# Kernel tuning notes

Hardware: AMD Instinct MI355X
Metric: run time of the kernel (lower is better)

Reference implementation:

```python
import jax, jax.numpy as jnp
import numpy as np

NUM_CLASSES = 1000
EMBED_DIM = 1024
BATCH = 32768
FACTOR = 0.3


def setup_inputs() -> dict:
    key = jax.random.key(0)
    k1, k2, k3 = jax.random.split(key, 3)
    embed = jax.random.normal(k1, (BATCH, EMBED_DIM), dtype=jnp.float32)
    y = jax.random.randint(k2, (BATCH,), 0, NUM_CLASSES, dtype=jnp.int64)
    centroid = jax.random.normal(k3, (NUM_CLASSES, EMBED_DIM), dtype=jnp.float32)
    return {"embed": embed, "y": y, "centroid": centroid}


def reference(embed, y, centroid):
    # Per-class sum of embeddings: equivalent to eye(C)[y].T @ embed,
    # done as a scatter-add (segment_sum) instead of a dense one-hot matmul.
    sums = jax.ops.segment_sum(embed, y, num_segments=NUM_CLASSES)  # [C, D]
    counts = jax.ops.segment_sum(
        jnp.ones((embed.shape[0],), dtype=embed.dtype), y, num_segments=NUM_CLASSES
    )  # [C] == weight.sum(dim=1)
    cur_centroid = sums / counts[:, None]  # per-class mean
    new_centroid = FACTOR * cur_centroid + (1.0 - FACTOR) * centroid
    return new_centroid
```

## Files before the change

kernel.cpp:

```cpp
#include <hip/hip_runtime.h>


#define BATCH       32768
#define EMBED_DIM   1024
#define NUM_CLASSES 1000
#define FACTOR      0.3f
#define MAX_ROWS    512

__global__ __launch_bounds__(256) void centroid_kernel(
    const float* __restrict__ embed,
    const int*   __restrict__ y,
    const float* __restrict__ centroid,
    float*       __restrict__ out)
{
    const int c   = blockIdx.x;
    const int tid = threadIdx.x;
    const int d0  = tid * 4;

    __shared__ int rows[MAX_ROWS];
    __shared__ int nmatch;

    if (tid == 0) nmatch = 0;

    const size_t o = (size_t)c * EMBED_DIM + d0;
    const float4 cen = *reinterpret_cast<const float4*>(centroid + o);

    __syncthreads();

    #pragma unroll 4
    for (int base = 0; base < BATCH; base += 1024) {
        const int idx = base + d0;
        const int4 v = *reinterpret_cast<const int4*>(y + idx);
        if (v.x == c) { int p = atomicAdd(&nmatch, 1); rows[p] = idx + 0; }
        if (v.y == c) { int p = atomicAdd(&nmatch, 1); rows[p] = idx + 1; }
        if (v.z == c) { int p = atomicAdd(&nmatch, 1); rows[p] = idx + 2; }
        if (v.w == c) { int p = atomicAdd(&nmatch, 1); rows[p] = idx + 3; }
    }
    __syncthreads();

    const int m = nmatch;

    float4 acc = make_float4(0.f, 0.f, 0.f, 0.f);
    int j = 0;
    for (; j + 8 <= m; j += 8) {
        float4 v[8];
        #pragma unroll
        for (int u = 0; u < 8; ++u) {
            const int r = rows[j + u];
            v[u] = *reinterpret_cast<const float4*>(
                embed + (size_t)r * EMBED_DIM + d0);
        }
        #pragma unroll
        for (int u = 0; u < 8; ++u) {
            acc.x += v[u].x; acc.y += v[u].y;
            acc.z += v[u].z; acc.w += v[u].w;
        }
    }
    for (; j < m; ++j) {
        const int r = rows[j];
        const float4 v = *reinterpret_cast<const float4*>(
            embed + (size_t)r * EMBED_DIM + d0);
        acc.x += v.x; acc.y += v.y; acc.z += v.z; acc.w += v.w;
    }

    const float inv = 1.0f / (float)m;
    float4 res;
    res.x = FACTOR * (acc.x * inv) + (1.0f - FACTOR) * cen.x;
    res.y = FACTOR * (acc.y * inv) + (1.0f - FACTOR) * cen.y;
    res.z = FACTOR * (acc.z * inv) + (1.0f - FACTOR) * cen.z;
    res.w = FACTOR * (acc.w * inv) + (1.0f - FACTOR) * cen.w;
    *reinterpret_cast<float4*>(out + o) = res;
}

extern "C" void kernel_launch(void* const* d_in, const int* in_sizes, int n_in,
                              void* d_out, int out_size, void* d_ws, size_t ws_size,
                              hipStream_t stream) {
    const float* embed    = (const float*)d_in[0];
    const int*   y        = (const int*)d_in[1];
    const float* centroid = (const float*)d_in[2];
    float*       out      = (float*)d_out;

    centroid_kernel<<<NUM_CLASSES, 256, 0, stream>>>(embed, y, centroid, out);
}
```

Measured before the change: 211.7 us.

## Process four classes per block to amortize label scan

Each block now scans the label array once and buckets matching rows for four consecutive classes into per-class shared lists. It then gathers and averages each class in turn. This cuts the number of full label-array scans by four, reducing redundant L2 traffic. The trade-off is a quarter as many blocks, which lowers occupancy and concurrency during the embedding gather.

```diff
diff --git a/kernel.cpp b/kernel.cpp
--- a/kernel.cpp
+++ b/kernel.cpp
@@ -5,7 +5,8 @@
 #define EMBED_DIM   1024
 #define NUM_CLASSES 1000
 #define FACTOR      0.3f
-#define MAX_ROWS    512
+#define G           4
+#define MAXR        256
 
 __global__ __launch_bounds__(256) void centroid_kernel(
     const float* __restrict__ embed,
@@ -13,63 +14,65 @@
     const float* __restrict__ centroid,
     float*       __restrict__ out)
 {
-    const int c   = blockIdx.x;
+    const int c0  = blockIdx.x * G;
     const int tid = threadIdx.x;
     const int d0  = tid * 4;
 
-    __shared__ int rows[MAX_ROWS];
-    __shared__ int nmatch;
+    __shared__ int rows[G][MAXR];
+    __shared__ int nm[G];
 
-    if (tid == 0) nmatch = 0;
-
-    const size_t o = (size_t)c * EMBED_DIM + d0;
-    const float4 cen = *reinterpret_cast<const float4*>(centroid + o);
-
+    if (tid < G) nm[tid] = 0;
     __syncthreads();
 
-    #pragma unroll 4
+    #pragma unroll 8
     for (int base = 0; base < BATCH; base += 1024) {
         const int idx = base + d0;
         const int4 v = *reinterpret_cast<const int4*>(y + idx);
-        if (v.x == c) { int p = atomicAdd(&nmatch, 1); rows[p] = idx + 0; }
-        if (v.y == c) { int p = atomicAdd(&nmatch, 1); rows[p] = idx + 1; }
-        if (v.z == c) { int p = atomicAdd(&nmatch, 1); rows[p] = idx + 2; }
-        if (v.w == c) { int p = atomicAdd(&nmatch, 1); rows[p] = idx + 3; }
+        unsigned u;
+        u = (unsigned)(v.x - c0); if (u < G) { int p = atomicAdd(&nm[u], 1); rows[u][p] = idx + 0; }
+        u = (unsigned)(v.y - c0); if (u < G) { int p = atomicAdd(&nm[u], 1); rows[u][p] = idx + 1; }
+        u = (unsigned)(v.z - c0); if (u < G) { int p = atomicAdd(&nm[u], 1); rows[u][p] = idx + 2; }
+        u = (unsigned)(v.w - c0); if (u < G) { int p = atomicAdd(&nm[u], 1); rows[u][p] = idx + 3; }
     }
     __syncthreads();
 
-    const int m = nmatch;
+    for (int g = 0; g < G; ++g) {
+        const int m = nm[g];
+        const int* rl = rows[g];
 
-    float4 acc = make_float4(0.f, 0.f, 0.f, 0.f);
-    int j = 0;
-    for (; j + 8 <= m; j += 8) {
-        float4 v[8];
-        #pragma unroll
-        for (int u = 0; u < 8; ++u) {
-            const int r = rows[j + u];
-            v[u] = *reinterpret_cast<const float4*>(
+        float4 acc = make_float4(0.f, 0.f, 0.f, 0.f);
+        int j = 0;
+        for (; j + 8 <= m; j += 8) {
+            float4 v[8];
+            #pragma unroll
+            for (int u = 0; u < 8; ++u) {
+                const int r = rl[j + u];
+                v[u] = *reinterpret_cast<const float4*>(
+                    embed + (size_t)r * EMBED_DIM + d0);
+            }
+            #pragma unroll
+            for (int u = 0; u < 8; ++u) {
+                acc.x += v[u].x; acc.y += v[u].y;
+                acc.z += v[u].z; acc.w += v[u].w;
+            }
+        }
+        for (; j < m; ++j) {
+            const int r = rl[j];
+            const float4 v = *reinterpret_cast<const float4*>(
                 embed + (size_t)r * EMBED_DIM + d0);
+            acc.x += v.x; acc.y += v.y; acc.z += v.z; acc.w += v.w;
         }
-        #pragma unroll
-        for (int u = 0; u < 8; ++u) {
-            acc.x += v[u].x; acc.y += v[u].y;
-            acc.z += v[u].z; acc.w += v[u].w;
-        }
+
+        const float inv = 1.0f / (float)m;
+        const size_t o = (size_t)(c0 + g) * EMBED_DIM + d0;
+        const float4 cen = *reinterpret_cast<const float4*>(centroid + o);
+        float4 res;
+        res.x = FACTOR * (acc.x * inv) + (1.0f - FACTOR) * cen.x;
+        res.y = FACTOR * (acc.y * inv) + (1.0f - FACTOR) * cen.y;
+        res.z = FACTOR * (acc.z * inv) + (1.0f - FACTOR) * cen.z;
+        res.w = FACTOR * (acc.w * inv) + (1.0f - FACTOR) * cen.w;
+        *reinterpret_cast<float4*>(out + o) = res;
     }
-    for (; j < m; ++j) {
-        const int r = rows[j];
-        const float4 v = *reinterpret_cast<const float4*>(
-            embed + (size_t)r * EMBED_DIM + d0);
-        acc.x += v.x; acc.y += v.y; acc.z += v.z; acc.w += v.w;
-    }
-
-    const float inv = 1.0f / (float)m;
-    float4 res;
-    res.x = FACTOR * (acc.x * inv) + (1.0f - FACTOR) * cen.x;
-    res.y = FACTOR * (acc.y * inv) + (1.0f - FACTOR) * cen.y;
-    res.z = FACTOR * (acc.z * inv) + (1.0f - FACTOR) * cen.z;
-    res.w = FACTOR * (acc.w * inv) + (1.0f - FACTOR) * cen.w;
-    *reinterpret_cast<float4*>(out + o) = res;
 }
 
 extern "C" void kernel_launch(void* const* d_in, const int* in_sizes, int n_in,
@@ -80,5 +83,5 @@
     const float* centroid = (const float*)d_in[2];
     float*       out      = (float*)d_out;
 
-    centroid_kernel<<<NUM_CLASSES, 256, 0, stream>>>(embed, y, centroid, out);
+    centroid_kernel<<<NUM_CLASSES / G, 256, 0, stream>>>(embed, y, centroid, out);
 }
```

After: 217.3 us. +2.7%, slower.

## Split each class across two blocks over embedding halves with padded unrolled gather

Applied to the files above, without the earlier changes.

Launches two blocks per class, each handling half of the embedding dimension with float2 loads. This doubles the grid to raise occupancy and memory-level parallelism. The row list is padded to a multiple of 16 with duplicates of row 0 so the gather loop has no remainder; the extra contribution is subtracted with an FMA afterwards. Four partial accumulators break the add dependency chain. The cost is that every block rescans all labels, doubling label-scan work. MAXR shrinks to 128, which overflows if any class gets more than 128 samples; with random labels a class averages about 33.

```diff
diff --git a/kernel.cpp b/kernel.cpp
--- a/kernel.cpp
+++ b/kernel.cpp
@@ -5,7 +5,8 @@
 #define EMBED_DIM   1024
 #define NUM_CLASSES 1000
 #define FACTOR      0.3f
-#define MAX_ROWS    512
+#define MAXR        128
+#define HALF_DIM    512
 
 __global__ __launch_bounds__(256) void centroid_kernel(
     const float* __restrict__ embed,
@@ -13,23 +14,25 @@
     const float* __restrict__ centroid,
     float*       __restrict__ out)
 {
-    const int c   = blockIdx.x;
+    const int bid = blockIdx.x;
+    const int c   = bid >> 1;
+    const int h   = bid & 1;
     const int tid = threadIdx.x;
-    const int d0  = tid * 4;
+    const int d0  = h * HALF_DIM + tid * 2;
 
-    __shared__ int rows[MAX_ROWS];
+    __shared__ int rows[MAXR];
     __shared__ int nmatch;
 
     if (tid == 0) nmatch = 0;
 
     const size_t o = (size_t)c * EMBED_DIM + d0;
-    const float4 cen = *reinterpret_cast<const float4*>(centroid + o);
+    const float2 cen = *reinterpret_cast<const float2*>(centroid + o);
 
     __syncthreads();
 
-    #pragma unroll 4
+    #pragma unroll 8
     for (int base = 0; base < BATCH; base += 1024) {
-        const int idx = base + d0;
+        const int idx = base + tid * 4;
         const int4 v = *reinterpret_cast<const int4*>(y + idx);
         if (v.x == c) { int p = atomicAdd(&nmatch, 1); rows[p] = idx + 0; }
         if (v.y == c) { int p = atomicAdd(&nmatch, 1); rows[p] = idx + 1; }
@@ -38,38 +41,49 @@
     }
     __syncthreads();
 
-    const int m = nmatch;
+    const int m  = nmatch;
+    const int mp = (m + 15) & ~15;
 
-    float4 acc = make_float4(0.f, 0.f, 0.f, 0.f);
-    int j = 0;
-    for (; j + 8 <= m; j += 8) {
-        float4 v[8];
+    if (tid >= m && tid < mp) rows[tid] = rows[0];
+    __syncthreads();
+
+    float2 accs[4];
+    #pragma unroll
+    for (int a = 0; a < 4; ++a) accs[a] = make_float2(0.f, 0.f);
+
+    for (int j = 0; j < mp; j += 16) {
+        float2 v[16];
         #pragma unroll
-        for (int u = 0; u < 8; ++u) {
+        for (int u = 0; u < 16; ++u) {
             const int r = rows[j + u];
-            v[u] = *reinterpret_cast<const float4*>(
+            v[u] = *reinterpret_cast<const float2*>(
                 embed + (size_t)r * EMBED_DIM + d0);
         }
         #pragma unroll
-        for (int u = 0; u < 8; ++u) {
-            acc.x += v[u].x; acc.y += v[u].y;
-            acc.z += v[u].z; acc.w += v[u].w;
+        for (int u = 0; u < 16; ++u) {
+            accs[u & 3].x += v[u].x;
+            accs[u & 3].y += v[u].y;
         }
     }
-    for (; j < m; ++j) {
-        const int r = rows[j];
-        const float4 v = *reinterpret_cast<const float4*>(
-            embed + (size_t)r * EMBED_DIM + d0);
-        acc.x += v.x; acc.y += v.y; acc.z += v.z; acc.w += v.w;
+
+    if (mp > m) {
+        const float pad = (float)(mp - m);
+        const int r0 = rows[0];
+        const float2 v0 = *reinterpret_cast<const float2*>(
+            embed + (size_t)r0 * EMBED_DIM + d0);
+        accs[0].x = fmaf(-pad, v0.x, accs[0].x);
+        accs[0].y = fmaf(-pad, v0.y, accs[0].y);
     }
 
+    float2 acc;
+    acc.x = (accs[0].x + accs[1].x) + (accs[2].x + accs[3].x);
+    acc.y = (accs[0].y + accs[1].y) + (accs[2].y + accs[3].y);
+
     const float inv = 1.0f / (float)m;
-    float4 res;
+    float2 res;
     res.x = FACTOR * (acc.x * inv) + (1.0f - FACTOR) * cen.x;
     res.y = FACTOR * (acc.y * inv) + (1.0f - FACTOR) * cen.y;
-    res.z = FACTOR * (acc.z * inv) + (1.0f - FACTOR) * cen.z;
-    res.w = FACTOR * (acc.w * inv) + (1.0f - FACTOR) * cen.w;
-    *reinterpret_cast<float4*>(out + o) = res;
+    *reinterpret_cast<float2*>(out + o) = res;
 }
 
 extern "C" void kernel_launch(void* const* d_in, const int* in_sizes, int n_in,
@@ -80,5 +94,5 @@
     const float* centroid = (const float*)d_in[2];
     float*       out      = (float*)d_out;
 
-    centroid_kernel<<<NUM_CLASSES, 256, 0, stream>>>(embed, y, centroid, out);
+    centroid_kernel<<<NUM_CLASSES * 2, 256, 0, stream>>>(embed, y, centroid, out);
 }
```

After: 212.9 us. No clear change (+0.6%).
